# Kernel optimization log

Hardware: AMD Instinct MI355X
Metric: run time of the kernel (lower is better)

Reference implementation:

```python
import jax, jax.numpy as jnp
import numpy as np
from jax import lax

IN_CH = 256
OUT_CH = 256
INTER = IN_CH // 2
KERNEL = 3


def setup_inputs() -> dict:
    key = jax.random.key(0)
    ks = jax.random.split(key, 6)
    B, C, H, W = 8, IN_CH, 128, 128
    x = jax.random.normal(ks[0], (B, C, H, W), dtype=jnp.float32)
    s = 1.0 / np.sqrt(C)
    Wq = jax.random.normal(ks[1], (INTER, C), dtype=jnp.float32) * s
    Wk = jax.random.normal(ks[2], (INTER, C), dtype=jnp.float32) * s
    Wv = jax.random.normal(ks[3], (INTER, C), dtype=jnp.float32) * s
    w1d = jax.random.normal(ks[4], (KERNEL,), dtype=jnp.float32) * (1.0 / np.sqrt(KERNEL))
    Wc = jax.random.normal(ks[5], (OUT_CH, INTER, 3, 3), dtype=jnp.float32) * (1.0 / np.sqrt(INTER * 9))
    return {"x": x, "Wq": Wq, "Wk": Wk, "Wv": Wv, "w1d": w1d, "Wc": Wc}


def reference(x, Wq, Wk, Wv, w1d, Wc):
    B, C, H, W = x.shape
    inter = Wq.shape[0]
    Hs, Ws = H // 4, W // 4  # 1x1 conv, stride 4, pad 0 == spatial subsample
    xs = x[:, :, ::4, ::4]  # [B, C, Hs, Ws]
    q = jnp.einsum('oc,bchw->bohw', Wq, xs).reshape(B, inter, Hs * Ws)  # [B, inter, N]
    k = jnp.einsum('oc,bchw->bohw', Wk, xs).reshape(B, inter, Hs * Ws)
    v = jnp.einsum('oc,bchw->bohw', Wv, xs).reshape(B, inter, Hs * Ws)
    # gate = softmax(Q^T K) over last dim, shape [B, N, N]
    scores = jnp.einsum('bcn,bcm->bnm', q, k)
    gate = jax.nn.softmax(scores, axis=-1)
    # gated value: [B, inter, N] -> [B, inter, Hs, Ws]
    gv = jnp.einsum('bnm,bcm->bcn', gate, v).reshape(B, inter, Hs, Ws)
    # ECA channel gating: global avg pool -> conv1d over channel dim -> sigmoid
    ca = gv.mean(axis=(2, 3))  # [B, inter]
    ca = lax.conv_general_dilated(
        ca[:, None, :],                     # [B, 1, inter]
        w1d[None, None, :],                 # [1, 1, K]
        window_strides=(1,), padding=[((KERNEL - 1) // 2,) * 2],
        dimension_numbers=('NCH', 'OIH', 'NCH'))
    ca = jax.nn.sigmoid(ca)[:, 0, :, None, None]  # [B, inter, 1, 1]
    out = gv * ca
    out = lax.conv_general_dilated(
        out, Wc, window_strides=(1, 1), padding='SAME',
        dimension_numbers=('NCHW', 'OIHW', 'NCHW'))
    return out, gate, ca
```

## Files before the change

### kernel.cpp

```cpp
#include <hip/hip_runtime.h>
#include <math.h>

#define B_   8
#define C_   256
#define CI_  128
#define N_   1024
#define HW_  32
#define CO_  256

typedef __bf16 v8bf __attribute__((ext_vector_type(8)));
typedef float  f32x4 __attribute__((ext_vector_type(4)));
typedef unsigned short ushort_t;

__device__ __forceinline__ unsigned short f2bf_rne(float f) {
    unsigned int u = __float_as_uint(f);
    unsigned int r = u + 0x7FFF + ((u >> 16) & 1);
    return (unsigned short)(r >> 16);
}
__device__ __forceinline__ float bf2f(unsigned short h) {
    return __uint_as_float(((unsigned int)h) << 16);
}
__device__ __forceinline__ v8bf ld8(const ushort_t* p) {
    return *(const v8bf*)p;
}

__global__ __launch_bounds__(256) void prep_all_kernel(
    const float* __restrict__ x,
    const float* __restrict__ Wc,
    const float* __restrict__ Wq, const float* __restrict__ Wk,
    const float* __restrict__ Wv,
    ushort_t* __restrict__ Whi, ushort_t* __restrict__ Wlo,
    ushort_t* __restrict__ Wp_hi, ushort_t* __restrict__ Wp_lo,
    ushort_t* __restrict__ xs_hi, ushort_t* __restrict__ xs_lo,
    float* __restrict__ meanb)
{
    __shared__ ushort_t lh[32 * 264];
    __shared__ ushort_t ll[32 * 264];
    const int bx = blockIdx.x;
    const int tid = threadIdx.x;

    if (bx < 1152) {
        if (bx == 0) {
            *(float4*)&meanb[tid * 4] = make_float4(0.f, 0.f, 0.f, 0.f);
        }
        int idx = bx * 256 + tid;
        int o = idx / 1152;
        int r = idx - o * 1152;
        int ci = r / 9;
        int tap = r - ci * 9;
        float v = Wc[idx];
        unsigned short h = f2bf_rne(v);
        unsigned short l = f2bf_rne(v - bf2f(h));
        int didx = o * 1152 + tap * 128 + ci;
        Whi[didx] = h; Wlo[didx] = l;
    } else if (bx < 1536) {
        int j = (bx - 1152) * 256 + tid;
        int o = j >> 8, c = j & 255;
        float v = (o < 128) ? Wq[o * 256 + c]
                : (o < 256) ? Wk[(o - 128) * 256 + c]
                            : Wv[(o - 256) * 256 + c];
        unsigned short h = f2bf_rne(v);
        unsigned short l = f2bf_rne(v - bf2f(h));
        Wp_hi[j] = h; Wp_lo[j] = l;
    } else {
        const int bx2 = bx - 1536;
        const int h = bx2 & 31, b = bx2 >> 5;
        const int w = tid & 31, cg = tid >> 5;
        float v[32];
        #pragma unroll
        for (int i = 0; i < 32; ++i) {
            int c = i * 8 + cg;
            v[i] = x[((size_t)(b * C_ + c) * 128 + h * 4) * 128 + w * 4];
        }
        #pragma unroll
        for (int i = 0; i < 32; ++i) {
            int c = i * 8 + cg;
            unsigned short hi = f2bf_rne(v[i]);
            unsigned short lo = f2bf_rne(v[i] - bf2f(hi));
            lh[w * 264 + c] = hi;
            ll[w * 264 + c] = lo;
        }
        __syncthreads();
        const int ww = tid >> 3, cs = tid & 7;
        size_t dst = ((size_t)(b * N_) + h * 32 + ww) * 256 + cs * 32;
        #pragma unroll
        for (int t = 0; t < 4; ++t) {
            *(uint4*)&xs_hi[dst + t * 8] = *(uint4*)&lh[ww * 264 + cs * 32 + t * 8];
            *(uint4*)&xs_lo[dst + t * 8] = *(uint4*)&ll[ww * 264 + cs * 32 + t * 8];
        }
    }
}

__global__ __launch_bounds__(256) void proj_mfma_kernel(
    const ushort_t* __restrict__ Wp_hi, const ushort_t* __restrict__ Wp_lo,
    const ushort_t* __restrict__ xs_hi, const ushort_t* __restrict__ xs_lo,
    ushort_t* __restrict__ qt_hi, ushort_t* __restrict__ qt_lo,
    ushort_t* __restrict__ kt_hi, ushort_t* __restrict__ kt_lo,
    ushort_t* __restrict__ vB_hi, ushort_t* __restrict__ vB_lo)
{
    const int lin = blockIdx.x + 16 * (blockIdx.y + 6 * blockIdx.z);
    const int b    = lin & 7;
    const int rest = lin >> 3;
    const int n0 = (rest & 15) * 64;
    const int o0 = (rest >> 4) * 64;
    const int tid = threadIdx.x;
    const int l = tid & 63, wv = tid >> 6;
    const int wy = wv >> 1, wx = wv & 1;
    const int ln = l & 15, quad = l >> 4;

    f32x4 acc[2][2];
    #pragma unroll
    for (int i = 0; i < 2; ++i)
        #pragma unroll
        for (int j = 0; j < 2; ++j) acc[i][j] = (f32x4){0.f,0.f,0.f,0.f};

    const ushort_t* Ah_p[2]; const ushort_t* Al_p[2];
    const ushort_t* Bh_p[2]; const ushort_t* Bl_p[2];
    #pragma unroll
    for (int i = 0; i < 2; ++i) {
        size_t off = (size_t)(o0 + wy * 32 + i * 16 + ln) * 256 + quad * 8;
        Ah_p[i] = Wp_hi + off; Al_p[i] = Wp_lo + off;
    }
    #pragma unroll
    for (int j = 0; j < 2; ++j) {
        size_t off = ((size_t)(b * N_) + n0 + wx * 32 + j * 16 + ln) * 256 + quad * 8;
        Bh_p[j] = xs_hi + off; Bl_p[j] = xs_lo + off;
    }

    #pragma unroll 4
    for (int k0 = 0; k0 < 256; k0 += 32) {
        v8bf Ah[2], Al[2], Bh[2], Bl[2];
        #pragma unroll
        for (int i = 0; i < 2; ++i) { Ah[i] = ld8(Ah_p[i] + k0); Al[i] = ld8(Al_p[i] + k0); }
        #pragma unroll
        for (int j = 0; j < 2; ++j) { Bh[j] = ld8(Bh_p[j] + k0); Bl[j] = ld8(Bl_p[j] + k0); }
        __builtin_amdgcn_s_setprio(1);
        #pragma unroll
        for (int i = 0; i < 2; ++i)
            #pragma unroll
            for (int j = 0; j < 2; ++j) {
                acc[i][j] = __builtin_amdgcn_mfma_f32_16x16x32_bf16(Ah[i], Bh[j], acc[i][j], 0, 0, 0);
                acc[i][j] = __builtin_amdgcn_mfma_f32_16x16x32_bf16(Ah[i], Bl[j], acc[i][j], 0, 0, 0);
                acc[i][j] = __builtin_amdgcn_mfma_f32_16x16x32_bf16(Al[i], Bh[j], acc[i][j], 0, 0, 0);
            }
        __builtin_amdgcn_s_setprio(0);
    }

    if (o0 < 256) {
        ushort_t* th = (o0 < 128) ? qt_hi : kt_hi;
        ushort_t* tl = (o0 < 128) ? qt_lo : kt_lo;
        const int ob = o0 & 127;
        #pragma unroll
        for (int i = 0; i < 2; ++i)
            #pragma unroll
            for (int j = 0; j < 2; ++j) {
                int oo = ob + wy * 32 + i * 16 + quad * 4;
                int n  = n0 + wx * 32 + j * 16 + ln;
                unsigned int h01 = 0, h23 = 0, l01 = 0, l23 = 0;
                #pragma unroll
                for (int r = 0; r < 4; ++r) {
                    float f = acc[i][j][r];
                    unsigned short hh = f2bf_rne(f);
                    unsigned short lo = f2bf_rne(f - bf2f(hh));
                    if (r < 2) { h01 |= ((unsigned)hh) << (16 * r); l01 |= ((unsigned)lo) << (16 * r); }
                    else       { h23 |= ((unsigned)hh) << (16 * (r - 2)); l23 |= ((unsigned)lo) << (16 * (r - 2)); }
                }
                size_t off = ((size_t)(b * N_) + n) * 128 + oo;
                *(uint2*)&th[off] = make_uint2(h01, h23);
                *(uint2*)&tl[off] = make_uint2(l01, l23);
            }
    } else {
        #pragma unroll
        for (int i = 0; i < 2; ++i)
            #pragma unroll
            for (int j = 0; j < 2; ++j)
                #pragma unroll
                for (int r = 0; r < 4; ++r) {
                    int c = (o0 - 256) + wy * 32 + i * 16 + quad * 4 + r;
                    int m = n0 + wx * 32 + j * 16 + ln;
                    float f = acc[i][j][r];
                    unsigned short hh = f2bf_rne(f);
                    unsigned short lo = f2bf_rne(f - bf2f(hh));
                    size_t off = (((size_t)b * 32 + (m >> 5)) * 128 + c) * 32 + (m & 31);
                    vB_hi[off] = hh; vB_lo[off] = lo;
                }
    }
}

__global__ __launch_bounds__(512, 2) void attn_fused_kernel(
    const ushort_t* __restrict__ qt_hi, const ushort_t* __restrict__ qt_lo,
    const ushort_t* __restrict__ kt_hi, const ushort_t* __restrict__ kt_lo,
    const ushort_t* __restrict__ vB_hi, const ushort_t* __restrict__ vB_lo,
    float* __restrict__ gate, float* __restrict__ gv, float* __restrict__ meanb)
{
    __shared__ __align__(16) char gsm[65536];
    __shared__ float redA[8][32];
    __shared__ float redB[8][32];

    const int lin = blockIdx.x + 32 * blockIdx.y;
    const int b  = lin & 7;
    const int n0 = (lin >> 3) * 32;
    const int tid = threadIdx.x;
    const int l = tid & 63, w = tid >> 6;
    const int ln = l & 15, quad = l >> 4;
    const int Mw = w * 128;

    const ushort_t* qb_h = qt_hi + ((size_t)(b * N_) + n0) * 128;
    const ushort_t* qb_l = qt_lo + ((size_t)(b * N_) + n0) * 128;
    const ushort_t* kb_h = kt_hi + (size_t)(b * N_) * 128;
    const ushort_t* kb_l = kt_lo + (size_t)(b * N_) * 128;

    f32x4 acc[2][8];
    #pragma unroll
    for (int nt = 0; nt < 2; ++nt)
        #pragma unroll
        for (int mt = 0; mt < 8; ++mt) acc[nt][mt] = (f32x4){0.f,0.f,0.f,0.f};

    #pragma unroll
    for (int c0 = 0; c0 < 128; c0 += 32) {
        v8bf Ah[2], Al[2];
        #pragma unroll
        for (int nt = 0; nt < 2; ++nt) {
            size_t aoff = (size_t)(nt * 16 + ln) * 128 + c0 + quad * 8;
            Ah[nt] = ld8(qb_h + aoff); Al[nt] = ld8(qb_l + aoff);
        }
        #pragma unroll
        for (int mt = 0; mt < 8; ++mt) {
            size_t boff = (size_t)(Mw + mt * 16 + ln) * 128 + c0 + quad * 8;
            v8bf Bh = ld8(kb_h + boff);
            v8bf Bl = ld8(kb_l + boff);
            __builtin_amdgcn_s_setprio(1);
            #pragma unroll
            for (int nt = 0; nt < 2; ++nt) {
                acc[nt][mt] = __builtin_amdgcn_mfma_f32_16x16x32_bf16(Ah[nt], Bh, acc[nt][mt], 0, 0, 0);
                acc[nt][mt] = __builtin_amdgcn_mfma_f32_16x16x32_bf16(Ah[nt], Bl, acc[nt][mt], 0, 0, 0);
                acc[nt][mt] = __builtin_amdgcn_mfma_f32_16x16x32_bf16(Al[nt], Bh, acc[nt][mt], 0, 0, 0);
            }
            __builtin_amdgcn_s_setprio(0);
        }
    }

    float rmax[2][4];
    #pragma unroll
    for (int nt = 0; nt < 2; ++nt)
        #pragma unroll
        for (int r = 0; r < 4; ++r) {
            float m = acc[nt][0][r];
            #pragma unroll
            for (int mt = 1; mt < 8; ++mt) m = fmaxf(m, acc[nt][mt][r]);
            rmax[nt][r] = m;
        }
    #pragma unroll
    for (int nt = 0; nt < 2; ++nt)
        #pragma unroll
        for (int r = 0; r < 4; ++r) {
            float m = rmax[nt][r];
            #pragma unroll
            for (int xm = 1; xm <= 8; xm <<= 1) m = fmaxf(m, __shfl_xor(m, xm, 64));
            rmax[nt][r] = m;
        }
    if (ln == 0) {
        #pragma unroll
        for (int nt = 0; nt < 2; ++nt)
            #pragma unroll
            for (int r = 0; r < 4; ++r)
                redA[w][nt * 16 + quad * 4 + r] = rmax[nt][r];
    }
    __syncthreads();
    #pragma unroll
    for (int nt = 0; nt < 2; ++nt)
        #pragma unroll
        for (int r = 0; r < 4; ++r) {
            int row = nt * 16 + quad * 4 + r;
            float m0 = fmaxf(fmaxf(redA[0][row], redA[1][row]),
                             fmaxf(redA[2][row], redA[3][row]));
            float m1 = fmaxf(fmaxf(redA[4][row], redA[5][row]),
                             fmaxf(redA[6][row], redA[7][row]));
            rmax[nt][r] = fmaxf(m0, m1);
        }

    float rsum[2][4];
    #pragma unroll
    for (int nt = 0; nt < 2; ++nt)
        #pragma unroll
        for (int r = 0; r < 4; ++r) {
            float s = 0.f;
            #pragma unroll
            for (int mt = 0; mt < 8; ++mt) {
                float e = __expf(acc[nt][mt][r] - rmax[nt][r]);
                acc[nt][mt][r] = e;
                s += e;
            }
            rsum[nt][r] = s;
        }
    #pragma unroll
    for (int nt = 0; nt < 2; ++nt)
        #pragma unroll
        for (int r = 0; r < 4; ++r) {
            float s = rsum[nt][r];
            #pragma unroll
            for (int xm = 1; xm <= 8; xm <<= 1) s += __shfl_xor(s, xm, 64);
            rsum[nt][r] = s;
        }
    if (ln == 0) {
        #pragma unroll
        for (int nt = 0; nt < 2; ++nt)
            #pragma unroll
            for (int r = 0; r < 4; ++r)
                redB[w][nt * 16 + quad * 4 + r] = rsum[nt][r];
    }
    __syncthreads();
    #pragma unroll
    for (int nt = 0; nt < 2; ++nt)
        #pragma unroll
        for (int r = 0; r < 4; ++r) {
            int row = nt * 16 + quad * 4 + r;
            float inv = 1.0f / ((redB[0][row] + redB[1][row] + redB[2][row] + redB[3][row]) +
                                (redB[4][row] + redB[5][row] + redB[6][row] + redB[7][row]));
            #pragma unroll
            for (int mt = 0; mt < 8; ++mt) acc[nt][mt][r] *= inv;
        }

    #pragma unroll
    for (int nt = 0; nt < 2; ++nt)
        #pragma unroll
        for (int r = 0; r < 4; ++r) {
            int nl = nt * 16 + quad * 4 + r;
            #pragma unroll
            for (int mt = 0; mt < 8; ++mt) {
                int m = Mw + mt * 16 + ln;
                int chunk = m >> 3;
                int addr = nl * 2048 + (((chunk ^ (nl & 7))) << 4) + ((m & 7) << 1);
                *(ushort_t*)&gsm[addr] = f2bf_rne(acc[nt][mt][r]);
            }
        }
    __syncthreads();

    const ushort_t* vb_h = vB_hi + (size_t)b * CI_ * N_;
    const ushort_t* vb_l = vB_lo + (size_t)b * CI_ * N_;

    f32x4 acc2[2];
    acc2[0] = (f32x4){0.f,0.f,0.f,0.f};
    acc2[1] = (f32x4){0.f,0.f,0.f,0.f};

    #pragma unroll 4
    for (int m0 = 0; m0 < 1024; m0 += 32) {
        v8bf Bg[2];
        #pragma unroll
        for (int nt = 0; nt < 2; ++nt) {
            int nl = nt * 16 + ln;
            int chunk = (m0 >> 3) + quad;
            Bg[nt] = *(const v8bf*)&gsm[nl * 2048 + (((chunk ^ (nl & 7))) << 4)];
        }
        int c = w * 16 + ln;
        size_t aoff = (((size_t)(m0 >> 5)) * 128 + c) * 32 + quad * 8;
        v8bf Avh = ld8(vb_h + aoff);
        v8bf Avl = ld8(vb_l + aoff);
        __builtin_amdgcn_s_setprio(1);
        #pragma unroll
        for (int nt = 0; nt < 2; ++nt) {
            acc2[nt] = __builtin_amdgcn_mfma_f32_16x16x32_bf16(Avh, Bg[nt], acc2[nt], 0, 0, 0);
            acc2[nt] = __builtin_amdgcn_mfma_f32_16x16x32_bf16(Avl, Bg[nt], acc2[nt], 0, 0, 0);
        }
        __builtin_amdgcn_s_setprio(0);
    }

    #pragma unroll
    for (int nt = 0; nt < 2; ++nt) {
        int n = n0 + nt * 16 + ln;
        float4 o4 = make_float4(acc2[nt][0], acc2[nt][1], acc2[nt][2], acc2[nt][3]);
        *(float4*)&gv[((size_t)(b * N_) + n) * CI_ + w * 16 + quad * 4] = o4;
    }

    float* grow = gate + (size_t)b * N_ * N_;
    #pragma unroll
    for (int nt = 0; nt < 2; ++nt)
        #pragma unroll
        for (int r = 0; r < 4; ++r) {
            int n = n0 + nt * 16 + quad * 4 + r;
            #pragma unroll
            for (int mt = 0; mt < 8; ++mt) {
                int m = Mw + mt * 16 + ln;
                grow[(size_t)n * N_ + m] = acc[nt][mt][r];
            }
        }

    float s0 = acc2[0][0] + acc2[1][0];
    float s1 = acc2[0][1] + acc2[1][1];
    float s2 = acc2[0][2] + acc2[1][2];
    float s3 = acc2[0][3] + acc2[1][3];
    #pragma unroll
    for (int xm = 1; xm <= 8; xm <<= 1) {
        s0 += __shfl_xor(s0, xm, 64);
        s1 += __shfl_xor(s1, xm, 64);
        s2 += __shfl_xor(s2, xm, 64);
        s3 += __shfl_xor(s3, xm, 64);
    }
    if (ln == 0) {
        int cb = b * CI_ + w * 16 + quad * 4;
        atomicAdd(&meanb[cb + 0], s0);
        atomicAdd(&meanb[cb + 1], s1);
        atomicAdd(&meanb[cb + 2], s2);
        atomicAdd(&meanb[cb + 3], s3);
    }
}

#define BHI  0
#define BLO  17408
__global__ __launch_bounds__(256) void conv_mfma_kernel(
    const float* __restrict__ gv, const float* __restrict__ meanb,
    const float* __restrict__ w1d,
    const ushort_t* __restrict__ Whi, const ushort_t* __restrict__ Wlo,
    float* __restrict__ ca_out, float* __restrict__ out)
{
    __shared__ __align__(16) char smem[67584];
    __shared__ float ca_s[128];
    const int AH[2] = {34816, 51200};
    const int AL[2] = {43008, 59392};

    const int lin = blockIdx.x + 4 * (blockIdx.y + 16 * blockIdx.z);
    const int b    = lin & 7;
    const int rest = lin >> 3;
    const int o0 = (rest & 3) * 64;
    const int h0 = (rest >> 2) * 2;
    const int tid = threadIdx.x;
    const int l   = tid & 63;
    const int wv  = tid >> 6;
    const int wy  = wv >> 1;
    const int wx  = wv & 1;
    const int ln  = l & 15;
    const int quad = l >> 4;

    if (tid < 128) {
        const float sc = 1.0f / 1024.0f;
        int t = b * 128 + tid;
        float left  = (tid > 0)   ? meanb[t - 1] * sc : 0.0f;
        float mid   = meanb[t] * sc;
        float right = (tid < 127) ? meanb[t + 1] * sc : 0.0f;
        float val = w1d[0] * left + w1d[1] * mid + w1d[2] * right;
        float s = 1.0f / (1.0f + __expf(-val));
        ca_s[tid] = s;
        if (rest == 0) ca_out[t] = s;
    }

    f32x4 acc[2][2];
    #pragma unroll
    for (int i = 0; i < 2; ++i)
        #pragma unroll
        for (int j = 0; j < 2; ++j)
            acc[i][j] = (f32x4){0.f, 0.f, 0.f, 0.f};

    const int srow0 = tid >> 3, scol = tid & 7;
    const int la0 = srow0 * 128 + scol * 16;
    const int la1 = (srow0 + 32) * 128 + scol * 16;

    for (int half = 0; half < 2; ++half) {
        __syncthreads();
        for (int u = tid; u < 136 * 16; u += 256) {
            int p   = u >> 4;
            int ciq = u & 15;
            int hrel = p / 34;
            int c    = p - hrel * 34;
            int gr = h0 + hrel - 1;
            int gc = c - 1;
            bool ok = ((unsigned)gr < 32u) && ((unsigned)gc < 32u);
            int cib = half * 64 + ciq * 4;
            float vv[4] = {0.f, 0.f, 0.f, 0.f};
            if (ok) {
                float4 v4 = *(const float4*)&gv[((size_t)(b * N_) + gr * 32 + gc) * CI_ + cib];
                float4 c4 = *(const float4*)&ca_s[cib];
                vv[0] = v4.x * c4.x; vv[1] = v4.y * c4.y;
                vv[2] = v4.z * c4.z; vv[3] = v4.w * c4.w;
            }
            unsigned int hx = 0, hy = 0, lx = 0, ly = 0;
            #pragma unroll
            for (int t = 0; t < 4; ++t) {
                unsigned short h = f2bf_rne(vv[t]);
                unsigned short lo = f2bf_rne(vv[t] - bf2f(h));
                if (t < 2) { hx |= ((unsigned)h) << (16 * t); lx |= ((unsigned)lo) << (16 * t); }
                else       { hy |= ((unsigned)h) << (16 * (t - 2)); ly |= ((unsigned)lo) << (16 * (t - 2)); }
            }
            int addr = p * 128 + (((ciq >> 1) ^ (p & 7)) << 4) + ((ciq & 1) << 3);
            *(uint2*)&smem[BHI + addr] = make_uint2(hx, hy);
            *(uint2*)&smem[BLO + addr] = make_uint2(lx, ly);
        }
        {
            int csrc0 = scol ^ (srow0 & 7);
            int csrc1 = scol ^ ((srow0 + 32) & 7);
            size_t g0 = (size_t)(o0 + srow0) * 1152 + half * 64 + csrc0 * 8;
            size_t g1 = (size_t)(o0 + srow0 + 32) * 1152 + half * 64 + csrc1 * 8;
            uint4 h0r = *(const uint4*)&Whi[g0];
            uint4 l0r = *(const uint4*)&Wlo[g0];
            uint4 h1r = *(const uint4*)&Whi[g1];
            uint4 l1r = *(const uint4*)&Wlo[g1];
            *(uint4*)&smem[AH[0] + la0] = h0r;
            *(uint4*)&smem[AL[0] + la0] = l0r;
            *(uint4*)&smem[AH[0] + la1] = h1r;
            *(uint4*)&smem[AL[0] + la1] = l1r;
        }

        for (int tap = 0; tap < 9; ++tap) {
            __syncthreads();
            uint4 nh0, nl0, nh1, nl1;
            if (tap < 8) {
                int ntap = tap + 1;
                int csrc0 = scol ^ (srow0 & 7);
                int csrc1 = scol ^ ((srow0 + 32) & 7);
                size_t g0 = (size_t)(o0 + srow0) * 1152 + ntap * 128 + half * 64 + csrc0 * 8;
                size_t g1 = (size_t)(o0 + srow0 + 32) * 1152 + ntap * 128 + half * 64 + csrc1 * 8;
                nh0 = *(const uint4*)&Whi[g0];
                nl0 = *(const uint4*)&Wlo[g0];
                nh1 = *(const uint4*)&Whi[g1];
                nl1 = *(const uint4*)&Wlo[g1];
            }
            const int ah = AH[tap & 1], al = AL[tap & 1];
            const int dy = tap / 3, dx = tap - dy * 3;
            const int pbase = (wx + dy) * 34 + dx;
            #pragma unroll
            for (int cc = 0; cc < 2; ++cc) {
                v8bf Bh[2], Bl[2], Ah2[2], Al2[2];
                #pragma unroll
                for (int j = 0; j < 2; ++j) {
                    int p = pbase + j * 16 + ln;
                    int ch = cc * 4 + quad;
                    int addr = p * 128 + ((ch ^ (p & 7)) << 4);
                    Bh[j] = *(const v8bf*)&smem[BHI + addr];
                    Bl[j] = *(const v8bf*)&smem[BLO + addr];
                }
                #pragma unroll
                for (int i = 0; i < 2; ++i) {
                    int o = wy * 32 + i * 16 + ln;
                    int ch = cc * 4 + quad;
                    int addr = o * 128 + ((ch ^ (o & 7)) << 4);
                    Ah2[i] = *(const v8bf*)&smem[ah + addr];
                    Al2[i] = *(const v8bf*)&smem[al + addr];
                }
                #pragma unroll
                for (int i = 0; i < 2; ++i)
                    #pragma unroll
                    for (int j = 0; j < 2; ++j) {
                        acc[i][j] = __builtin_amdgcn_mfma_f32_16x16x32_bf16(Ah2[i], Bh[j], acc[i][j], 0, 0, 0);
                        acc[i][j] = __builtin_amdgcn_mfma_f32_16x16x32_bf16(Ah2[i], Bl[j], acc[i][j], 0, 0, 0);
                        acc[i][j] = __builtin_amdgcn_mfma_f32_16x16x32_bf16(Al2[i], Bh[j], acc[i][j], 0, 0, 0);
                    }
            }
            if (tap < 8) {
                int nb = (tap + 1) & 1;
                *(uint4*)&smem[AH[nb] + la0] = nh0;
                *(uint4*)&smem[AL[nb] + la0] = nl0;
                *(uint4*)&smem[AH[nb] + la1] = nh1;
                *(uint4*)&smem[AL[nb] + la1] = nl1;
            }
        }
    }

    const int h = h0 + wx;
    #pragma unroll
    for (int i = 0; i < 2; ++i)
        #pragma unroll
        for (int j = 0; j < 2; ++j)
            #pragma unroll
            for (int r = 0; r < 4; ++r) {
                int o = o0 + wy * 32 + i * 16 + quad * 4 + r;
                int w = j * 16 + ln;
                out[(size_t)(b * CO_ + o) * N_ + h * 32 + w] = acc[i][j][r];
            }
}

extern "C" void kernel_launch(void* const* d_in, const int* in_sizes, int n_in,
                              void* d_out, int out_size, void* d_ws, size_t ws_size,
                              hipStream_t stream) {
    const float* x   = (const float*)d_in[0];
    const float* Wq  = (const float*)d_in[1];
    const float* Wk  = (const float*)d_in[2];
    const float* Wv  = (const float*)d_in[3];
    const float* w1d = (const float*)d_in[4];
    const float* Wc  = (const float*)d_in[5];

    float* out  = (float*)d_out;
    float* gate = out + 2097152;
    float* ca   = gate + 8388608;

    float*    gv      = (float*)d_ws;
    float*    meanb   = gv + 1048576;
    ushort_t* Whi     = (ushort_t*)(meanb + 1024);
    ushort_t* Wlo     = Whi + 294912;
    ushort_t* Wp_hi   = Wlo + 294912;
    ushort_t* Wp_lo   = Wp_hi + 98304;
    ushort_t* xs_hi   = Wp_lo + 98304;
    ushort_t* xs_lo   = xs_hi + 2097152;
    ushort_t* qt_hi   = xs_lo + 2097152;
    ushort_t* qt_lo   = qt_hi + 1048576;
    ushort_t* kt_hi   = qt_lo + 1048576;
    ushort_t* kt_lo   = kt_hi + 1048576;
    ushort_t* vB_hi   = kt_lo + 1048576;
    ushort_t* vB_lo   = vB_hi + 1048576;

    prep_all_kernel<<<dim3(1792), 256, 0, stream>>>(
        x, Wc, Wq, Wk, Wv, Whi, Wlo, Wp_hi, Wp_lo, xs_hi, xs_lo, meanb);
    proj_mfma_kernel<<<dim3(16, 6, 8), 256, 0, stream>>>(
        Wp_hi, Wp_lo, xs_hi, xs_lo, qt_hi, qt_lo, kt_hi, kt_lo, vB_hi, vB_lo);
    attn_fused_kernel<<<dim3(32, 8), 512, 0, stream>>>(
        qt_hi, qt_lo, kt_hi, kt_lo, vB_hi, vB_lo, gate, gv, meanb);
    conv_mfma_kernel<<<dim3(4, 16, 8), 256, 0, stream>>>(
        gv, meanb, w1d, Whi, Wlo, ca, out);
}
```

Measured before the change: 284.0 us.

## Precompute scaled bf16 hi/lo gv in separate kernel, split x-subsample prep, vectorize V stores

Moves the ECA gate computation and the scaling plus hi/lo bf16 split of gv into a new gvca_prep_kernel. The conv kernel then loads pre-split bf16 halos with 16-byte loads instead of redoing the fp32 conversion for each halo tile. Prep of the subsampled x is split across four times more blocks, each with a smaller LDS footprint. The V projection swaps its MFMA operand order so the transposed vB layout can be written with packed uint2 stores, and conv MFMAs gain setprio hints. In exchange this adds a kernel launch and an extra round trip of gv through global memory.

Result: faster. 276.0 us (-2.8%).

```diff
diff --git a/kernel.cpp b/kernel.cpp
--- a/kernel.cpp
+++ b/kernel.cpp
@@ -34,8 +34,8 @@
     ushort_t* __restrict__ xs_hi, ushort_t* __restrict__ xs_lo,
     float* __restrict__ meanb)
 {
-    __shared__ ushort_t lh[32 * 264];
-    __shared__ ushort_t ll[32 * 264];
+    __shared__ ushort_t lh[32 * 72];
+    __shared__ ushort_t ll[32 * 72];
     const int bx = blockIdx.x;
     const int tid = threadIdx.x;
 
@@ -64,30 +64,29 @@
         Wp_hi[j] = h; Wp_lo[j] = l;
     } else {
         const int bx2 = bx - 1536;
-        const int h = bx2 & 31, b = bx2 >> 5;
+        const int cq = bx2 & 3;
+        const int h  = (bx2 >> 2) & 31;
+        const int b  = bx2 >> 7;
         const int w = tid & 31, cg = tid >> 5;
-        float v[32];
-        #pragma unroll
-        for (int i = 0; i < 32; ++i) {
-            int c = i * 8 + cg;
+        float v[8];
+        #pragma unroll
+        for (int i = 0; i < 8; ++i) {
+            int c = cq * 64 + i * 8 + cg;
             v[i] = x[((size_t)(b * C_ + c) * 128 + h * 4) * 128 + w * 4];
         }
         #pragma unroll
-        for (int i = 0; i < 32; ++i) {
-            int c = i * 8 + cg;
+        for (int i = 0; i < 8; ++i) {
+            int cl = i * 8 + cg;
             unsigned short hi = f2bf_rne(v[i]);
             unsigned short lo = f2bf_rne(v[i] - bf2f(hi));
-            lh[w * 264 + c] = hi;
-            ll[w * 264 + c] = lo;
+            lh[w * 72 + cl] = hi;
+            ll[w * 72 + cl] = lo;
         }
         __syncthreads();
         const int ww = tid >> 3, cs = tid & 7;
-        size_t dst = ((size_t)(b * N_) + h * 32 + ww) * 256 + cs * 32;
-        #pragma unroll
-        for (int t = 0; t < 4; ++t) {
-            *(uint4*)&xs_hi[dst + t * 8] = *(uint4*)&lh[ww * 264 + cs * 32 + t * 8];
-            *(uint4*)&xs_lo[dst + t * 8] = *(uint4*)&ll[ww * 264 + cs * 32 + t * 8];
-        }
+        size_t dst = ((size_t)(b * N_) + h * 32 + ww) * 256 + cq * 64 + cs * 8;
+        *(uint4*)&xs_hi[dst] = *(uint4*)&lh[ww * 72 + cs * 8];
+        *(uint4*)&xs_lo[dst] = *(uint4*)&ll[ww * 72 + cs * 8];
     }
 }
 
@@ -108,12 +107,6 @@
     const int wy = wv >> 1, wx = wv & 1;
     const int ln = l & 15, quad = l >> 4;
 
-    f32x4 acc[2][2];
-    #pragma unroll
-    for (int i = 0; i < 2; ++i)
-        #pragma unroll
-        for (int j = 0; j < 2; ++j) acc[i][j] = (f32x4){0.f,0.f,0.f,0.f};
-
     const ushort_t* Ah_p[2]; const ushort_t* Al_p[2];
     const ushort_t* Bh_p[2]; const ushort_t* Bl_p[2];
     #pragma unroll
@@ -127,26 +120,31 @@
         Bh_p[j] = xs_hi + off; Bl_p[j] = xs_lo + off;
     }
 
-    #pragma unroll 4
-    for (int k0 = 0; k0 < 256; k0 += 32) {
-        v8bf Ah[2], Al[2], Bh[2], Bl[2];
-        #pragma unroll
-        for (int i = 0; i < 2; ++i) { Ah[i] = ld8(Ah_p[i] + k0); Al[i] = ld8(Al_p[i] + k0); }
-        #pragma unroll
-        for (int j = 0; j < 2; ++j) { Bh[j] = ld8(Bh_p[j] + k0); Bl[j] = ld8(Bl_p[j] + k0); }
-        __builtin_amdgcn_s_setprio(1);
-        #pragma unroll
-        for (int i = 0; i < 2; ++i)
-            #pragma unroll
-            for (int j = 0; j < 2; ++j) {
-                acc[i][j] = __builtin_amdgcn_mfma_f32_16x16x32_bf16(Ah[i], Bh[j], acc[i][j], 0, 0, 0);
-                acc[i][j] = __builtin_amdgcn_mfma_f32_16x16x32_bf16(Ah[i], Bl[j], acc[i][j], 0, 0, 0);
-                acc[i][j] = __builtin_amdgcn_mfma_f32_16x16x32_bf16(Al[i], Bh[j], acc[i][j], 0, 0, 0);
-            }
-        __builtin_amdgcn_s_setprio(0);
-    }
+    f32x4 acc[2][2];
+    #pragma unroll
+    for (int i = 0; i < 2; ++i)
+        #pragma unroll
+        for (int j = 0; j < 2; ++j) acc[i][j] = (f32x4){0.f,0.f,0.f,0.f};
 
     if (o0 < 256) {
+        #pragma unroll 4
+        for (int k0 = 0; k0 < 256; k0 += 32) {
+            v8bf Ah[2], Al[2], Bh[2], Bl[2];
+            #pragma unroll
+            for (int i = 0; i < 2; ++i) { Ah[i] = ld8(Ah_p[i] + k0); Al[i] = ld8(Al_p[i] + k0); }
+            #pragma unroll
+            for (int j = 0; j < 2; ++j) { Bh[j] = ld8(Bh_p[j] + k0); Bl[j] = ld8(Bl_p[j] + k0); }
+            __builtin_amdgcn_s_setprio(1);
+            #pragma unroll
+            for (int i = 0; i < 2; ++i)
+                #pragma unroll
+                for (int j = 0; j < 2; ++j) {
+                    acc[i][j] = __builtin_amdgcn_mfma_f32_16x16x32_bf16(Ah[i], Bh[j], acc[i][j], 0, 0, 0);
+                    acc[i][j] = __builtin_amdgcn_mfma_f32_16x16x32_bf16(Ah[i], Bl[j], acc[i][j], 0, 0, 0);
+                    acc[i][j] = __builtin_amdgcn_mfma_f32_16x16x32_bf16(Al[i], Bh[j], acc[i][j], 0, 0, 0);
+                }
+            __builtin_amdgcn_s_setprio(0);
+        }
         ushort_t* th = (o0 < 128) ? qt_hi : kt_hi;
         ushort_t* tl = (o0 < 128) ? qt_lo : kt_lo;
         const int ob = o0 & 127;
@@ -170,20 +168,44 @@
                 *(uint2*)&tl[off] = make_uint2(l01, l23);
             }
     } else {
-        #pragma unroll
-        for (int i = 0; i < 2; ++i)
+        #pragma unroll 4
+        for (int k0 = 0; k0 < 256; k0 += 32) {
+            v8bf Ah[2], Al[2], Bh[2], Bl[2];
+            #pragma unroll
+            for (int i = 0; i < 2; ++i) { Ah[i] = ld8(Ah_p[i] + k0); Al[i] = ld8(Al_p[i] + k0); }
+            #pragma unroll
+            for (int j = 0; j < 2; ++j) { Bh[j] = ld8(Bh_p[j] + k0); Bl[j] = ld8(Bl_p[j] + k0); }
+            __builtin_amdgcn_s_setprio(1);
             #pragma unroll
             for (int j = 0; j < 2; ++j)
                 #pragma unroll
+                for (int i = 0; i < 2; ++i) {
+                    acc[j][i] = __builtin_amdgcn_mfma_f32_16x16x32_bf16(Bh[j], Ah[i], acc[j][i], 0, 0, 0);
+                    acc[j][i] = __builtin_amdgcn_mfma_f32_16x16x32_bf16(Bh[j], Al[i], acc[j][i], 0, 0, 0);
+                    acc[j][i] = __builtin_amdgcn_mfma_f32_16x16x32_bf16(Bl[j], Ah[i], acc[j][i], 0, 0, 0);
+                }
+            __builtin_amdgcn_s_setprio(0);
+        }
+        const int mhi = (n0 >> 5) + wx;
+        #pragma unroll
+        for (int j = 0; j < 2; ++j)
+            #pragma unroll
+            for (int i = 0; i < 2; ++i) {
+                int c   = (o0 - 256) + wy * 32 + i * 16 + ln;
+                int mlo = j * 16 + quad * 4;
+                unsigned int h01 = 0, h23 = 0, l01 = 0, l23 = 0;
+                #pragma unroll
                 for (int r = 0; r < 4; ++r) {
-                    int c = (o0 - 256) + wy * 32 + i * 16 + quad * 4 + r;
-                    int m = n0 + wx * 32 + j * 16 + ln;
-                    float f = acc[i][j][r];
+                    float f = acc[j][i][r];
                     unsigned short hh = f2bf_rne(f);
                     unsigned short lo = f2bf_rne(f - bf2f(hh));
-                    size_t off = (((size_t)b * 32 + (m >> 5)) * 128 + c) * 32 + (m & 31);
-                    vB_hi[off] = hh; vB_lo[off] = lo;
+                    if (r < 2) { h01 |= ((unsigned)hh) << (16 * r); l01 |= ((unsigned)lo) << (16 * r); }
+                    else       { h23 |= ((unsigned)hh) << (16 * (r - 2)); l23 |= ((unsigned)lo) << (16 * (r - 2)); }
                 }
+                size_t off = (((size_t)b * 32 + mhi) * 128 + c) * 32 + mlo;
+                *(uint2*)&vB_hi[off] = make_uint2(h01, h23);
+                *(uint2*)&vB_lo[off] = make_uint2(l01, l23);
+            }
     }
 }
 
@@ -405,16 +427,61 @@
     }
 }
 
+__global__ __launch_bounds__(256) void gvca_prep_kernel(
+    const float* __restrict__ gv, const float* __restrict__ meanb,
+    const float* __restrict__ w1d,
+    ushort_t* __restrict__ gvh, ushort_t* __restrict__ gvl,
+    float* __restrict__ ca_out)
+{
+    __shared__ float ca_s[128];
+    const int lin = blockIdx.x;
+    const int b  = lin & 7;
+    const int ns = lin >> 3;
+    const int tid = threadIdx.x;
+
+    if (tid < 128) {
+        const float sc = 1.0f / 1024.0f;
+        int t = b * 128 + tid;
+        float left  = (tid > 0)   ? meanb[t - 1] * sc : 0.0f;
+        float mid   = meanb[t] * sc;
+        float right = (tid < 127) ? meanb[t + 1] * sc : 0.0f;
+        float val = w1d[0] * left + w1d[1] * mid + w1d[2] * right;
+        float s = 1.0f / (1.0f + __expf(-val));
+        ca_s[tid] = s;
+        if (ns == 0) ca_out[t] = s;
+    }
+    __syncthreads();
+
+    const int cl = (tid & 31) * 4;
+    const int nr = tid >> 5;
+    #pragma unroll
+    for (int i = 0; i < 4; ++i) {
+        int n = ns * 32 + nr + i * 8;
+        size_t off = ((size_t)(b * N_) + n) * 128 + cl;
+        float4 v4 = *(const float4*)&gv[off];
+        float vv[4] = { v4.x * ca_s[cl], v4.y * ca_s[cl + 1],
+                        v4.z * ca_s[cl + 2], v4.w * ca_s[cl + 3] };
+        unsigned int h01 = 0, h23 = 0, l01 = 0, l23 = 0;
+        #pragma unroll
+        for (int t = 0; t < 4; ++t) {
+            unsigned short h = f2bf_rne(vv[t]);
+            unsigned short lo = f2bf_rne(vv[t] - bf2f(h));
+            if (t < 2) { h01 |= ((unsigned)h) << (16 * t); l01 |= ((unsigned)lo) << (16 * t); }
+            else       { h23 |= ((unsigned)h) << (16 * (t - 2)); l23 |= ((unsigned)lo) << (16 * (t - 2)); }
+        }
+        *(uint2*)&gvh[off] = make_uint2(h01, h23);
+        *(uint2*)&gvl[off] = make_uint2(l01, l23);
+    }
+}
+
 #define BHI  0
 #define BLO  17408
 __global__ __launch_bounds__(256) void conv_mfma_kernel(
-    const float* __restrict__ gv, const float* __restrict__ meanb,
-    const float* __restrict__ w1d,
+    const ushort_t* __restrict__ gvh, const ushort_t* __restrict__ gvl,
     const ushort_t* __restrict__ Whi, const ushort_t* __restrict__ Wlo,
-    float* __restrict__ ca_out, float* __restrict__ out)
+    float* __restrict__ out)
 {
     __shared__ __align__(16) char smem[67584];
-    __shared__ float ca_s[128];
     const int AH[2] = {34816, 51200};
     const int AL[2] = {43008, 59392};
 
@@ -431,18 +498,6 @@
     const int ln  = l & 15;
     const int quad = l >> 4;
 
-    if (tid < 128) {
-        const float sc = 1.0f / 1024.0f;
-        int t = b * 128 + tid;
-        float left  = (tid > 0)   ? meanb[t - 1] * sc : 0.0f;
-        float mid   = meanb[t] * sc;
-        float right = (tid < 127) ? meanb[t + 1] * sc : 0.0f;
-        float val = w1d[0] * left + w1d[1] * mid + w1d[2] * right;
-        float s = 1.0f / (1.0f + __expf(-val));
-        ca_s[tid] = s;
-        if (rest == 0) ca_out[t] = s;
-    }
-
     f32x4 acc[2][2];
     #pragma unroll
     for (int i = 0; i < 2; ++i)
@@ -456,33 +511,23 @@
 
     for (int half = 0; half < 2; ++half) {
         __syncthreads();
-        for (int u = tid; u < 136 * 16; u += 256) {
-            int p   = u >> 4;
-            int ciq = u & 15;
+        for (int u = tid; u < 136 * 8; u += 256) {
+            int p  = u >> 3;
+            int cs = u & 7;
             int hrel = p / 34;
             int c    = p - hrel * 34;
             int gr = h0 + hrel - 1;
             int gc = c - 1;
             bool ok = ((unsigned)gr < 32u) && ((unsigned)gc < 32u);
-            int cib = half * 64 + ciq * 4;
-            float vv[4] = {0.f, 0.f, 0.f, 0.f};
+            uint4 h4 = make_uint4(0, 0, 0, 0), l4 = make_uint4(0, 0, 0, 0);
             if (ok) {
-                float4 v4 = *(const float4*)&gv[((size_t)(b * N_) + gr * 32 + gc) * CI_ + cib];
-                float4 c4 = *(const float4*)&ca_s[cib];
-                vv[0] = v4.x * c4.x; vv[1] = v4.y * c4.y;
-                vv[2] = v4.z * c4.z; vv[3] = v4.w * c4.w;
-            }
-            unsigned int hx = 0, hy = 0, lx = 0, ly = 0;
-            #pragma unroll
-            for (int t = 0; t < 4; ++t) {
-                unsigned short h = f2bf_rne(vv[t]);
-                unsigned short lo = f2bf_rne(vv[t] - bf2f(h));
-                if (t < 2) { hx |= ((unsigned)h) << (16 * t); lx |= ((unsigned)lo) << (16 * t); }
-                else       { hy |= ((unsigned)h) << (16 * (t - 2)); ly |= ((unsigned)lo) << (16 * (t - 2)); }
-            }
-            int addr = p * 128 + (((ciq >> 1) ^ (p & 7)) << 4) + ((ciq & 1) << 3);
-            *(uint2*)&smem[BHI + addr] = make_uint2(hx, hy);
-            *(uint2*)&smem[BLO + addr] = make_uint2(lx, ly);
+                size_t src = ((size_t)(b * N_) + gr * 32 + gc) * 128 + half * 64 + cs * 8;
+                h4 = *(const uint4*)&gvh[src];
+                l4 = *(const uint4*)&gvl[src];
+            }
+            int addr = p * 128 + ((cs ^ (p & 7)) << 4);
+            *(uint4*)&smem[BHI + addr] = h4;
+            *(uint4*)&smem[BLO + addr] = l4;
         }
         {
             int csrc0 = scol ^ (srow0 & 7);
@@ -535,6 +580,7 @@
                     Ah2[i] = *(const v8bf*)&smem[ah + addr];
                     Al2[i] = *(const v8bf*)&smem[al + addr];
                 }
+                __builtin_amdgcn_s_setprio(1);
                 #pragma unroll
                 for (int i = 0; i < 2; ++i)
                     #pragma unroll
@@ -543,6 +589,7 @@
                         acc[i][j] = __builtin_amdgcn_mfma_f32_16x16x32_bf16(Ah2[i], Bl[j], acc[i][j], 0, 0, 0);
                         acc[i][j] = __builtin_amdgcn_mfma_f32_16x16x32_bf16(Al2[i], Bh[j], acc[i][j], 0, 0, 0);
                     }
+                __builtin_amdgcn_s_setprio(0);
             }
             if (tap < 8) {
                 int nb = (tap + 1) & 1;
@@ -595,13 +642,17 @@
     ushort_t* kt_lo   = kt_hi + 1048576;
     ushort_t* vB_hi   = kt_lo + 1048576;
     ushort_t* vB_lo   = vB_hi + 1048576;
-
-    prep_all_kernel<<<dim3(1792), 256, 0, stream>>>(
+    ushort_t* gvh     = vB_lo + 1048576;
+    ushort_t* gvl     = gvh + 1048576;
+
+    prep_all_kernel<<<dim3(2560), 256, 0, stream>>>(
         x, Wc, Wq, Wk, Wv, Whi, Wlo, Wp_hi, Wp_lo, xs_hi, xs_lo, meanb);
     proj_mfma_kernel<<<dim3(16, 6, 8), 256, 0, stream>>>(
         Wp_hi, Wp_lo, xs_hi, xs_lo, qt_hi, qt_lo, kt_hi, kt_lo, vB_hi, vB_lo);
     attn_fused_kernel<<<dim3(32, 8), 512, 0, stream>>>(
         qt_hi, qt_lo, kt_hi, kt_lo, vB_hi, vB_lo, gate, gv, meanb);
+    gvca_prep_kernel<<<dim3(256), 256, 0, stream>>>(
+        gv, meanb, w1d, gvh, gvl, ca);
     conv_mfma_kernel<<<dim3(4, 16, 8), 256, 0, stream>>>(
-        gv, meanb, w1d, Whi, Wlo, ca, out);
-}
+        gvh, gvl, Whi, Wlo, out);
+}
```
